# Optimization experiments

Measured on AMD Instinct MI355X. Metric: run time of the kernel, lower is better.

The kernel has to match this reference:

```python
import jax, jax.numpy as jnp
import numpy as np

THR = 1.0      # snntorch Leaky default threshold
SLOPE = 25.0   # surrogate.fast_sigmoid default slope
BETA = 0.5
NIN, NH1, NH2, NOUT = 6, 500, 500, 2

@jax.custom_vjp
def spike(x):
    # Heaviside forward, fast-sigmoid surrogate backward
    return (x > 0).astype(x.dtype)

def _spike_fwd(x):
    return spike(x), x

def _spike_bwd(x, g):
    return (g / (SLOPE * jnp.abs(x) + 1.0) ** 2,)

spike.defvjp(_spike_fwd, _spike_bwd)

def _lif(cur, mem):
    # snntorch Leaky (reset_mechanism='subtract'):
    # reset spike computed from previous membrane, then leaky integrate, then fire
    reset = spike(mem - THR)
    mem_new = BETA * mem + cur - reset * THR
    spk = spike(mem_new - THR)
    return spk, mem_new

def setup_inputs() -> dict:
    key = jax.random.key(0)
    ks = jax.random.split(key, 7)
    T, B = 500, 128
    x = jax.random.normal(ks[0], (T, B, NIN), jnp.float32)
    s1 = 1.0 / np.sqrt(NIN)
    s2 = 1.0 / np.sqrt(NH1)
    W1 = jax.random.uniform(ks[1], (NH1, NIN), jnp.float32, -s1, s1)
    b1 = jax.random.uniform(ks[2], (NH1,), jnp.float32, -s1, s1)
    W2 = jax.random.uniform(ks[3], (NH2, NH1), jnp.float32, -s2, s2)
    b2 = jax.random.uniform(ks[4], (NH2,), jnp.float32, -s2, s2)
    Wout = jax.random.uniform(ks[5], (NOUT, NH2), jnp.float32, -s2, s2)
    bout = jax.random.uniform(ks[6], (NOUT,), jnp.float32, -s2, s2)
    return {"x": x, "W1": W1, "b1": b1, "W2": W2, "b2": b2, "Wout": Wout, "bout": bout}

def reference(x, W1, b1, W2, b2, Wout, bout):
    B = x.shape[1]
    mem0 = (jnp.zeros((B, NH1), x.dtype),
            jnp.zeros((B, NH2), x.dtype),
            jnp.zeros((B, NOUT), x.dtype))

    def step(carry, xt):
        m1, m2, m3 = carry
        s1, m1 = _lif(xt @ W1.T + b1, m1)
        s2, m2 = _lif(s1 @ W2.T + b2, m2)
        s3, m3 = _lif(s2 @ Wout.T + bout, m3)
        return (m1, m2, m3), (s3, m3)

    _, (spk_rec, mem_rec) = jax.lax.scan(step, mem0, x)
    return spk_rec, mem_rec  # each [T, B, 2]
```

## Files before the change

### kernel.cpp

```cpp
#include <hip/hip_runtime.h>

#define T_STEPS 500
#define BATCH   128
#define NINPUT  6
#define NH      500
#define THRV    1.0f
#define BETAV   0.5f
#define W2T_STRIDE 512
#define NGC     8
#define JC      256
#define KT      128

typedef unsigned long long ull;

static __device__ __forceinline__ ull rfl64(ull v) {
  unsigned lo = __builtin_amdgcn_readfirstlane((unsigned)v);
  unsigned hi = __builtin_amdgcn_readfirstlane((unsigned)(v >> 32));
  return ((ull)hi << 32) | lo;
}

__global__ void transpose_w2(const float* __restrict__ W2, float* __restrict__ W2T) {
  int idx = blockIdx.x * 256 + threadIdx.x;
  if (idx < NH * W2T_STRIDE) {
    int i = idx >> 9;
    int j = idx & 511;
    W2T[idx] = (j < NH) ? W2[j * NH + i] : 0.f;
  }
}

#define PEEL4(mm, roff, A) do {                                               \
  ull m_ = (mm);                                                              \
  while (m_) {                                                                \
    int i0 = __builtin_ctzll(m_); m_ &= m_ - 1;                               \
    bool v1 = (m_ != 0); int i1 = v1 ? __builtin_ctzll(m_) : i0;              \
    if (v1) m_ &= m_ - 1;                                                     \
    bool v2 = (m_ != 0); int i2 = v2 ? __builtin_ctzll(m_) : i0;              \
    if (v2) m_ &= m_ - 1;                                                     \
    bool v3 = (m_ != 0); int i3 = v3 ? __builtin_ctzll(m_) : i0;              \
    if (v3) m_ &= m_ - 1;                                                     \
    float4 w0_ = W2L[(((roff) + i0) << 6) + lane];                            \
    float4 w1_ = W2L[(((roff) + i1) << 6) + lane];                            \
    float4 w2_ = W2L[(((roff) + i2) << 6) + lane];                            \
    float4 w3_ = W2L[(((roff) + i3) << 6) + lane];                            \
    A.x += w0_.x; A.y += w0_.y; A.z += w0_.z; A.w += w0_.w;                   \
    if (v1) { A.x += w1_.x; A.y += w1_.y; A.z += w1_.z; A.w += w1_.w; }       \
    if (v2) { A.x += w2_.x; A.y += w2_.y; A.z += w2_.z; A.w += w2_.w; }       \
    if (v3) { A.x += w3_.x; A.y += w3_.y; A.z += w3_.z; A.w += w3_.w; }       \
  }                                                                           \
} while (0)

__global__ __launch_bounds__(1024, 4) void fused_kernel(
    const float* __restrict__ x,
    const float* __restrict__ W1,
    const float* __restrict__ b1,
    const float* __restrict__ W2T,
    const float* __restrict__ b2,
    ull* __restrict__ s1seg,
    ull* __restrict__ s2seg)
{
  __shared__ __align__(16) char arena[131072];
  float4* W2L  = (float4*)arena;
  float*  SBUF = (float*)arena;
  float*  xs   = (float*)(arena + 131072 - T_STEPS * NINPUT * 4);

  const int b = blockIdx.x, jc = blockIdx.y;
  const int tid = threadIdx.x;
  const int lane = tid & 63, wid = tid >> 6;

  for (int idx = tid; idx < T_STEPS * NINPUT; idx += 1024) {
    int t = idx / NINPUT, k = idx - t * NINPUT;
    xs[idx] = x[(size_t)(t * BATCH + b) * NINPUT + k];
  }
  __syncthreads();

  if (wid < 8) {
    const int n = (wid << 6) + lane;
    const bool nv = (n < NH);
    float w[6], b1v;
    #pragma unroll
    for (int k = 0; k < 6; ++k) w[k] = nv ? W1[n * NINPUT + k] : 0.f;
    b1v = nv ? b1[n] : 0.f;
    float m1 = 0.f;

    #define LOADL(hh, xr) do {                                 \
      const float* p_ = xs + (hh) * NINPUT;                    \
      float2 a_ = *(const float2*)p_;                          \
      float2 c_ = *(const float2*)(p_ + 2);                    \
      float2 d_ = *(const float2*)(p_ + 4);                    \
      xr[0]=a_.x; xr[1]=a_.y; xr[2]=c_.x;                      \
      xr[3]=c_.y; xr[4]=d_.x; xr[5]=d_.y;                      \
    } while (0)

    float X0[6], X1[6], X2[6];
    LOADL(0, X0);
    LOADL(1, X1);
    for (int h = 0; h < T_STEPS; ++h) {
      int hp = h + 2; if (hp > T_STEPS - 1) hp = T_STEPS - 1;
      LOADL(hp, X2);
      float cur = b1v + w[0]*X0[0] + w[1]*X0[1] + w[2]*X0[2]
                      + w[3]*X0[3] + w[4]*X0[4] + w[5]*X0[5];
      float rst = (m1 > THRV) ? THRV : 0.f;
      m1 = BETAV * m1 + cur - rst;
      ull bm = __ballot((m1 > THRV) && nv);
      if (lane == 0) s1seg[((size_t)h * BATCH + b) * 8 + wid] = bm;
      #pragma unroll
      for (int k = 0; k < 6; ++k) { X0[k] = X1[k]; X1[k] = X2[k]; }
    }
    #undef LOADL
  }
  __syncthreads();

  const int j0 = jc * JC + (lane << 2);
  const bool jv4 = (j0 < NH);
  float4 b2v = make_float4(0.f, 0.f, 0.f, 0.f);
  if (jv4) b2v = *(const float4*)(b2 + j0);

  const int jg = jc * 256 + tid;
  const bool jvs = (jg < NH);
  const int word = jc * 4 + (tid >> 6);
  float m2 = 0.f;

  for (int r = 0; r < 4; ++r) {
    float4 acc[8];
    #pragma unroll
    for (int g = 0; g < 8; ++g) acc[g] = make_float4(0.f, 0.f, 0.f, 0.f);

    for (int kt = 0; kt < 4; ++kt) {
      __syncthreads();
      for (int idx = tid; idx < KT * (JC / 4); idx += 1024) {
        int rr = idx >> 6, cc = idx & 63;
        int grow = kt * KT + rr;
        float4 v = make_float4(0.f, 0.f, 0.f, 0.f);
        if (grow < NH)
          v = *(const float4*)(W2T + (size_t)grow * W2T_STRIDE + jc * JC + (cc << 2));
        W2L[idx] = v;
      }
      __syncthreads();

      ull qA[8], qB[8];
      #pragma unroll
      for (int g = 0; g < 8; ++g) {
        int h = r * 128 + g * 16 + wid;
        if (h < T_STEPS) {
          const ull* mp = s1seg + ((size_t)h * BATCH + b) * 8 + 2 * kt;
          qA[g] = mp[0]; qB[g] = mp[1];
        } else { qA[g] = 0; qB[g] = 0; }
      }
      #pragma unroll
      for (int g = 0; g < 8; ++g) {
        ull mA = rfl64(qA[g]);
        ull mB = rfl64(qB[g]);
        PEEL4(mA, 0,  acc[g]);
        PEEL4(mB, 64, acc[g]);
      }
    }

    __syncthreads();
    #pragma unroll
    for (int g = 0; g < 8; ++g) {
      float4 v = make_float4(acc[g].x + b2v.x, acc[g].y + b2v.y,
                             acc[g].z + b2v.z, acc[g].w + b2v.w);
      *(float4*)&SBUF[(size_t)(g * 16 + wid) * 256 + (lane << 2)] = v;
    }
    __syncthreads();

    if (tid < 256) {
      #pragma unroll 4
      for (int hl = 0; hl < 128; ++hl) {
        int h = r * 128 + hl;
        if (h < T_STEPS) {
          float v = SBUF[hl * 256 + tid];
          float rst = (m2 > THRV) ? THRV : 0.f;
          m2 = BETAV * m2 + v - rst;
          ull bm = __ballot((m2 > THRV) && jvs);
          if (lane == 0) s2seg[((size_t)h * BATCH + b) * 8 + word] = bm;
        }
      }
    }
  }
}

__global__ __launch_bounds__(256) void cur3_seg_kernel(
    const ull* __restrict__ s2seg,
    const float* __restrict__ Wout,
    float* __restrict__ cur3T)
{
  const int wid  = threadIdx.x >> 6;
  const int lane = threadIdx.x & 63;
  const int pl = blockIdx.x * 4 + wid;
  if (pl >= T_STEPS * BATCH) return;
  const int h  = pl >> 7;
  const int bb = pl & 127;

  float wa[NGC], wb[NGC];
  #pragma unroll
  for (int g = 0; g < NGC; ++g) {
    int j = g * 64 + lane;
    wa[g] = (j < NH) ? Wout[j] : 0.f;
    wb[g] = (j < NH) ? Wout[NH + j] : 0.f;
  }

  const ull* p = s2seg + (size_t)pl * 8;
  float c0 = 0.f, c1 = 0.f;
  #pragma unroll
  for (int g = 0; g < NGC; ++g) {
    ull mg = p[g];
    if ((mg >> lane) & 1ull) { c0 += wa[g]; c1 += wb[g]; }
  }
  #pragma unroll
  for (int off = 32; off; off >>= 1) {
    c0 += __shfl_xor(c0, off);
    c1 += __shfl_xor(c1, off);
  }
  if (lane == 0)
    *(float2*)(cur3T + ((size_t)bb * 512 + h) * 2) = make_float2(c0, c1);
}

__global__ __launch_bounds__(64) void scan3_kernel(
    const float* __restrict__ cur3T,
    const float* __restrict__ bout,
    float* __restrict__ out)
{
  const int b = blockIdx.x;
  const int lane = threadIdx.x;
  const float bo0 = bout[0], bo1 = bout[1];
  float m0 = 0.f, m1v = 0.f;

  float2 cur = *(const float2*)(cur3T + ((size_t)b * 512 + lane) * 2);

  for (int tcc = 0; tcc < T_STEPS; tcc += 64) {
    int tn = tcc + 64 + lane; if (tn > T_STEPS - 1) tn = T_STEPS - 1;
    float2 nxt = *(const float2*)(cur3T + ((size_t)b * 512 + tn) * 2);

    float c0 = cur.x + bo0, c1 = cur.y + bo1;
    int nsteps = T_STEPS - tcc; if (nsteps > 64) nsteps = 64;
    for (int k = 0; k < nsteps; ++k) {
      float cc0 = __shfl(c0, k);
      float cc1 = __shfl(c1, k);
      float r0 = (m0  > THRV) ? THRV : 0.f;
      float r1 = (m1v > THRV) ? THRV : 0.f;
      m0  = BETAV * m0  + cc0 - r0;
      m1v = BETAV * m1v + cc1 - r1;
      if (lane == k) {
        int t = tcc + k;
        size_t o = (size_t)(t * BATCH + b) * 2;
        out[o]     = (m0  > THRV) ? 1.f : 0.f;
        out[o + 1] = (m1v > THRV) ? 1.f : 0.f;
        out[(size_t)T_STEPS * BATCH * 2 + o]     = m0;
        out[(size_t)T_STEPS * BATCH * 2 + o + 1] = m1v;
      }
    }
    cur = nxt;
  }
}

extern "C" void kernel_launch(void* const* d_in, const int* in_sizes, int n_in,
                              void* d_out, int out_size, void* d_ws, size_t ws_size,
                              hipStream_t stream) {
  const float* x    = (const float*)d_in[0];
  const float* W1   = (const float*)d_in[1];
  const float* b1   = (const float*)d_in[2];
  const float* W2   = (const float*)d_in[3];
  const float* b2   = (const float*)d_in[4];
  const float* Wout = (const float*)d_in[5];
  const float* bout = (const float*)d_in[6];
  float* out = (float*)d_out;

  size_t off = 0;
  char* base = (char*)d_ws;
  auto carve = [&](size_t bytes) -> char* {
    char* r = base + off;
    off += (bytes + 511) & ~(size_t)511;
    return r;
  };
  float* W2T   = (float*)carve((size_t)NH * W2T_STRIDE * 4);
  ull*   s1seg = (ull*)carve((size_t)T_STEPS * BATCH * 8 * 8);
  ull*   s2seg = (ull*)carve((size_t)T_STEPS * BATCH * 8 * 8);
  float* cur3T = (float*)carve((size_t)BATCH * 512 * 2 * 4);

  transpose_w2<<<(NH * W2T_STRIDE + 255) / 256, 256, 0, stream>>>(W2, W2T);
  fused_kernel<<<dim3(BATCH, 2), 1024, 0, stream>>>(x, W1, b1, W2T, b2, s1seg, s2seg);
  cur3_seg_kernel<<<(T_STEPS * BATCH + 3) / 4, 256, 0, stream>>>(s2seg, Wout, cur3T);
  scan3_kernel<<<BATCH, 64, 0, stream>>>(cur3T, bout, out);
}
```

Measured before the change: 335.9 us.

## Batch spike-mask stores across 64 steps and stage W2 tiles via global_load_lds

Each lane now holds the ballot mask for one timestep, so a wave writes 64 steps of spike masks at once instead of lane 0 storing every step. This applies to both layer 1 and layer 2. The W2 tile copy into shared memory uses direct global-to-LDS 16-byte loads, with padded rows clamped to a valid row; those rows meet only zero spike bits, so results are unchanged. The layer-1 input prefetch is restructured into a 4-way rotating unrolled buffer. The batched stores are scattered across strided addresses, and the direct LDS loads depend on gfx950 support for 16-byte transfers.

Result: faster. 311.1 us (median of 2 runs) (-7.4%).

```diff
diff --git a/kernel.cpp b/kernel.cpp
--- a/kernel.cpp
+++ b/kernel.cpp
@@ -18,6 +18,10 @@
   unsigned hi = __builtin_amdgcn_readfirstlane((unsigned)(v >> 32));
   return ((ull)hi << 32) | lo;
 }
+
+#define GLDS16(gp, lp) __builtin_amdgcn_global_load_lds(                      \
+    (const __attribute__((address_space(1))) void*)(gp),                      \
+    (__attribute__((address_space(3))) void*)(lp), 16, 0, 0)
 
 __global__ void transpose_w2(const float* __restrict__ W2, float* __restrict__ W2T) {
   int idx = blockIdx.x * 256 + threadIdx.x;
@@ -81,6 +85,7 @@
     for (int k = 0; k < 6; ++k) w[k] = nv ? W1[n * NINPUT + k] : 0.f;
     b1v = nv ? b1[n] : 0.f;
     float m1 = 0.f;
+    ull keep1 = 0;
 
     #define LOADL(hh, xr) do {                                 \
       const float* p_ = xs + (hh) * NINPUT;                    \
@@ -91,21 +96,32 @@
       xr[3]=c_.y; xr[4]=d_.x; xr[5]=d_.y;                      \
     } while (0)
 
-    float X0[6], X1[6], X2[6];
-    LOADL(0, X0);
-    LOADL(1, X1);
-    for (int h = 0; h < T_STEPS; ++h) {
-      int hp = h + 2; if (hp > T_STEPS - 1) hp = T_STEPS - 1;
-      LOADL(hp, X2);
-      float cur = b1v + w[0]*X0[0] + w[1]*X0[1] + w[2]*X0[2]
-                      + w[3]*X0[3] + w[4]*X0[4] + w[5]*X0[5];
-      float rst = (m1 > THRV) ? THRV : 0.f;
-      m1 = BETAV * m1 + cur - rst;
-      ull bm = __ballot((m1 > THRV) && nv);
-      if (lane == 0) s1seg[((size_t)h * BATCH + b) * 8 + wid] = bm;
+    float X[4][6];
+    LOADL(0, X[0]);
+    LOADL(1, X[1]);
+    LOADL(2, X[2]);
+    LOADL(3, X[3]);
+
+    for (int h = 0; h < T_STEPS; h += 4) {
       #pragma unroll
-      for (int k = 0; k < 6; ++k) { X0[k] = X1[k]; X1[k] = X2[k]; }
-    }
+      for (int u = 0; u < 4; ++u) {
+        int hh = h + u;
+        if (hh < T_STEPS) {
+          float cur = b1v + w[0]*X[u][0] + w[1]*X[u][1] + w[2]*X[u][2]
+                          + w[3]*X[u][3] + w[4]*X[u][4] + w[5]*X[u][5];
+          float rst = (m1 > THRV) ? THRV : 0.f;
+          m1 = BETAV * m1 + cur - rst;
+          ull bm = __ballot((m1 > THRV) && nv);
+          keep1 = (lane == (hh & 63)) ? bm : keep1;
+          if ((hh & 63) == 63)
+            s1seg[((size_t)((hh - 63) + lane) * BATCH + b) * 8 + wid] = keep1;
+          int hp = hh + 4; if (hp > T_STEPS - 1) hp = T_STEPS - 1;
+          LOADL(hp, X[u]);
+        }
+      }
+    }
+    if (lane < (T_STEPS - 448))
+      s1seg[((size_t)(448 + lane) * BATCH + b) * 8 + wid] = keep1;
     #undef LOADL
   }
   __syncthreads();
@@ -119,6 +135,7 @@
   const bool jvs = (jg < NH);
   const int word = jc * 4 + (tid >> 6);
   float m2 = 0.f;
+  ull keep2 = 0;
 
   for (int r = 0; r < 4; ++r) {
     float4 acc[8];
@@ -127,13 +144,14 @@
 
     for (int kt = 0; kt < 4; ++kt) {
       __syncthreads();
-      for (int idx = tid; idx < KT * (JC / 4); idx += 1024) {
-        int rr = idx >> 6, cc = idx & 63;
+      #pragma unroll
+      for (int q = 0; q < 8; ++q) {
+        int flat = tid + q * 1024;
+        int rr = flat >> 6, cc = flat & 63;
         int grow = kt * KT + rr;
-        float4 v = make_float4(0.f, 0.f, 0.f, 0.f);
-        if (grow < NH)
-          v = *(const float4*)(W2T + (size_t)grow * W2T_STRIDE + jc * JC + (cc << 2));
-        W2L[idx] = v;
+        int growc = (grow < NH) ? grow : (NH - 1);
+        const float* gsrc = W2T + (size_t)growc * W2T_STRIDE + jc * JC + (cc << 2);
+        GLDS16(gsrc, &W2L[flat]);
       }
       __syncthreads();
 
@@ -173,11 +191,15 @@
           float rst = (m2 > THRV) ? THRV : 0.f;
           m2 = BETAV * m2 + v - rst;
           ull bm = __ballot((m2 > THRV) && jvs);
-          if (lane == 0) s2seg[((size_t)h * BATCH + b) * 8 + word] = bm;
+          keep2 = (lane == (h & 63)) ? bm : keep2;
+          if ((h & 63) == 63)
+            s2seg[((size_t)((h - 63) + lane) * BATCH + b) * 8 + word] = keep2;
         }
       }
     }
   }
+  if (tid < 256 && lane < (T_STEPS - 448))
+    s2seg[((size_t)(448 + lane) * BATCH + b) * 8 + word] = keep2;
 }
 
 __global__ __launch_bounds__(256) void cur3_seg_kernel(
```
